# Optimization experiments

Hardware: AMD Instinct MI355X
Metric: run time of the kernel (lower is better)

The kernel has to match this reference:

```python
import jax, jax.numpy as jnp
import numpy as np


def setup_inputs() -> dict:
    key = jax.random.key(0)
    k1, k2 = jax.random.split(key)
    B, T, C = 16, 4096, 1024
    x = jax.random.normal(k1, (B, T, C), dtype=jnp.float32)
    raw = jax.random.normal(k2, (C,), dtype=jnp.float32)
    return {"x": x, "raw": raw}


def reference(x, raw):
    # x: [B, T, C]; raw: [C] learnable logits -> alpha = sigmoid(raw)
    a = jax.nn.sigmoid(raw)            # [C]
    one_minus_a = 1.0 - a
    y0 = x[:, 0, :]                     # y_0 = x_0 (original initializes with raw first step)

    def step(y_prev, x_t):
        y_t = a * x_t + one_minus_a * y_prev
        return y_t, y_t

    xs = jnp.moveaxis(x[:, 1:, :], 1, 0)   # [T-1, B, C], scan over time
    _, ys = jax.lax.scan(step, y0, xs)      # ys: [T-1, B, C]
    y = jnp.concatenate([y0[:, None, :], jnp.moveaxis(ys, 0, 1)], axis=1)  # [B, T, C]
    return y
```

## Files before the change

### kernel.cpp

```cpp
#include <hip/hip_runtime.h>
#include <math.h>


#define T_DIM 4096
#define C_DIM 1024
#define CG    64
#define NWAVE 16
#define LSUB  16
#define TILE_T (NWAVE * LSUB)
#define NTILES (T_DIM / TILE_T)

__global__ __launch_bounds__(1024, 1)
void ema_scan_kernel(const float* __restrict__ x,
                     const float* __restrict__ raw,
                     float* __restrict__ y) {
    __shared__ float carry_lds[NWAVE][CG];

    const int lane = threadIdx.x & (CG - 1);
    const int w    = threadIdx.x >> 6;
    const int cg   = blockIdx.x;
    const int b    = blockIdx.y;
    const int c    = cg * CG + lane;

    const float rv = raw[c];
    const float a  = 1.0f / (1.0f + expf(-rv));
    const float d  = 1.0f - a;
    const float d2 = d * d, d4 = d2 * d2, d8 = d4 * d4;
    const float d16 = d8 * d8;

    const size_t base = ((size_t)b * T_DIM) * (size_t)C_DIM + (size_t)c;

    float run = 0.0f;

    for (int tile = 0; tile < NTILES; ++tile) {
        const int t0 = tile * TILE_T + w * LSUB;
        const float* xp = x + base + (size_t)t0 * C_DIM;

        float xv[LSUB];
        #pragma unroll
        for (int i = 0; i < LSUB; ++i) xv[i] = xp[(size_t)i * C_DIM];

        float yl[LSUB];
        float s = 0.0f;
        if (tile == 0 && w == 0) {
            s = xv[0];
            yl[0] = s;
            #pragma unroll
            for (int i = 1; i < LSUB; ++i) { s = fmaf(a, xv[i], d * s); yl[i] = s; }
        } else {
            #pragma unroll
            for (int i = 0; i < LSUB; ++i) { s = fmaf(a, xv[i], d * s); yl[i] = s; }
        }

        carry_lds[w][lane] = s;
        __syncthreads();

        float acc = run;
        float cin = 0.0f;
        #pragma unroll
        for (int j = 0; j < NWAVE; ++j) {
            if (j == w) cin = acc;
            acc = fmaf(d16, acc, carry_lds[j][lane]);
        }
        run = acc;
        __syncthreads();

        float* yp = y + base + (size_t)t0 * C_DIM;
        float f = d;
        #pragma unroll
        for (int i = 0; i < LSUB; ++i) {
            yp[(size_t)i * C_DIM] = fmaf(f, cin, yl[i]);
            f *= d;
        }
    }
}

extern "C" void kernel_launch(void* const* d_in, const int* in_sizes, int n_in,
                              void* d_out, int out_size, void* d_ws, size_t ws_size,
                              hipStream_t stream) {
    const float* x   = (const float*)d_in[0];
    const float* raw = (const float*)d_in[1];
    float* y = (float*)d_out;

    dim3 grid(C_DIM / CG, 16);
    dim3 block(1024);
    ema_scan_kernel<<<grid, block, 0, stream>>>(x, raw, y);
}
```

Baseline: 442.1 us.

## Vectorize EMA scan with float4 and double-buffer tile loads across iterations

Threads now process four channels each with float4 loads and stores, and blocks shrink to 256 threads over 32 channels, which gives 512 blocks instead of 256. The next tile's loads are issued before the barrier, and the carry buffer in shared memory alternates between two slots so only one barrier is needed per tile. The intent is to raise memory-level parallelism and cut synchronization on a bandwidth-bound scan. In exchange the sequential carry chain grows to 32 rows per tile, and holding three float4 arrays raises register pressure.

```diff
diff --git a/kernel.cpp b/kernel.cpp
--- a/kernel.cpp
+++ b/kernel.cpp
@@ -2,77 +2,107 @@
 #include <math.h>
 
 
-#define T_DIM 4096
-#define C_DIM 1024
-#define CG    64
-#define NWAVE 16
-#define LSUB  16
-#define TILE_T (NWAVE * LSUB)
+#define B_DIM  16
+#define T_DIM  4096
+#define C_DIM  1024
+#define CG     32
+#define COLS   8
+#define NROW   32
+#define LSUB   8
+#define TILE_T (NROW * LSUB)
 #define NTILES (T_DIM / TILE_T)
+#define TSTR   (C_DIM / 4)
 
-__global__ __launch_bounds__(1024, 1)
+__device__ __forceinline__ float4 f4mul(float4 a, float4 b) {
+    float4 r; r.x = a.x*b.x; r.y = a.y*b.y; r.z = a.z*b.z; r.w = a.w*b.w; return r;
+}
+__device__ __forceinline__ float4 f4fma(float4 a, float4 b, float4 c) {
+    float4 r;
+    r.x = fmaf(a.x, b.x, c.x); r.y = fmaf(a.y, b.y, c.y);
+    r.z = fmaf(a.z, b.z, c.z); r.w = fmaf(a.w, b.w, c.w); return r;
+}
+
+__global__ __launch_bounds__(256, 2)
 void ema_scan_kernel(const float* __restrict__ x,
                      const float* __restrict__ raw,
                      float* __restrict__ y) {
-    __shared__ float carry_lds[NWAVE][CG];
+    __shared__ float4 carry[2][NROW][COLS];
 
-    const int lane = threadIdx.x & (CG - 1);
-    const int w    = threadIdx.x >> 6;
-    const int cg   = blockIdx.x;
-    const int b    = blockIdx.y;
-    const int c    = cg * CG + lane;
+    const int tid = threadIdx.x;
+    const int col = tid & (COLS - 1);
+    const int row = tid >> 3;
+    const int cg  = blockIdx.x;
+    const int b   = blockIdx.y;
+    const int c0  = cg * CG + col * 4;
 
-    const float rv = raw[c];
-    const float a  = 1.0f / (1.0f + expf(-rv));
-    const float d  = 1.0f - a;
-    const float d2 = d * d, d4 = d2 * d2, d8 = d4 * d4;
-    const float d16 = d8 * d8;
+    const float4 rv = *reinterpret_cast<const float4*>(raw + c0);
+    float4 a, d, d8;
+    a.x = 1.0f / (1.0f + expf(-rv.x));
+    a.y = 1.0f / (1.0f + expf(-rv.y));
+    a.z = 1.0f / (1.0f + expf(-rv.z));
+    a.w = 1.0f / (1.0f + expf(-rv.w));
+    d.x = 1.0f - a.x; d.y = 1.0f - a.y; d.z = 1.0f - a.z; d.w = 1.0f - a.w;
+    float4 d2 = f4mul(d, d), d4 = f4mul(d2, d2);
+    d8 = f4mul(d4, d4);
 
-    const size_t base = ((size_t)b * T_DIM) * (size_t)C_DIM + (size_t)c;
+    const size_t chanBase = ((size_t)b * T_DIM) * C_DIM + (size_t)c0;
+    const float4* xb = reinterpret_cast<const float4*>(x + chanBase);
+    float4*       yb = reinterpret_cast<float4*>(y + chanBase);
 
-    float run = 0.0f;
+    float4 run = {0.f, 0.f, 0.f, 0.f};
+    float4 xvA[LSUB], xvB[LSUB], yl[LSUB];
 
-    for (int tile = 0; tile < NTILES; ++tile) {
-        const int t0 = tile * TILE_T + w * LSUB;
-        const float* xp = x + base + (size_t)t0 * C_DIM;
+#define LOADT(XV, tt) {                                                        \
+    const float4* p = xb + (size_t)((tt) * TILE_T + row * LSUB) * TSTR;        \
+    _Pragma("unroll")                                                          \
+    for (int i = 0; i < LSUB; ++i) XV[i] = p[(size_t)i * TSTR]; }
 
-        float xv[LSUB];
-        #pragma unroll
-        for (int i = 0; i < LSUB; ++i) xv[i] = xp[(size_t)i * C_DIM];
+#define BODY(XC, XN, tt, pb, doload) {                                         \
+                   \
+    float4 s;                                                                  \
+    if ((tt) == 0 && row == 0) {                                               \
+        s = XC[0]; yl[0] = s;                 \
+        _Pragma("unroll")                                                      \
+        for (int i = 1; i < LSUB; ++i) { s = f4fma(d, s, f4mul(a, XC[i])); yl[i] = s; } \
+    } else {                                                                   \
+        s.x = s.y = s.z = s.w = 0.f;                                           \
+        _Pragma("unroll")                                                      \
+        for (int i = 0; i < LSUB; ++i) { s = f4fma(d, s, f4mul(a, XC[i])); yl[i] = s; } \
+    }                                                                          \
+                                                 \
+    carry[pb][row][col] = s;                                                   \
+     \
+    if (doload) LOADT(XN, (tt) + 1);                                           \
+       \
+    asm volatile("s_waitcnt lgkmcnt(0)" ::: "memory");                         \
+    __builtin_amdgcn_s_barrier();                                              \
+    asm volatile("" ::: "memory");                                             \
+                \
+    float4 acc = run;                                                          \
+    float4 cin = {0.f, 0.f, 0.f, 0.f};                                         \
+    _Pragma("unroll 8")                                                        \
+    for (int j = 0; j < NROW; ++j) {                                           \
+        float4 cj = carry[pb][j][col];                                         \
+        if (j == row) cin = acc;                                               \
+        acc = f4fma(d8, acc, cj);                                              \
+    }                                                                          \
+    run = acc;                                                                 \
+                     \
+    float4* q = yb + (size_t)((tt) * TILE_T + row * LSUB) * TSTR;              \
+    float4 f = d;                                                              \
+    _Pragma("unroll")                                                          \
+    for (int i = 0; i < LSUB; ++i) {                                           \
+        q[(size_t)i * TSTR] = f4fma(f, cin, yl[i]);                            \
+        f = f4mul(f, d);                                                       \
+    } }
 
-        float yl[LSUB];
-        float s = 0.0f;
-        if (tile == 0 && w == 0) {
-            s = xv[0];
-            yl[0] = s;
-            #pragma unroll
-            for (int i = 1; i < LSUB; ++i) { s = fmaf(a, xv[i], d * s); yl[i] = s; }
-        } else {
-            #pragma unroll
-            for (int i = 0; i < LSUB; ++i) { s = fmaf(a, xv[i], d * s); yl[i] = s; }
-        }
-
-        carry_lds[w][lane] = s;
-        __syncthreads();
-
-        float acc = run;
-        float cin = 0.0f;
-        #pragma unroll
-        for (int j = 0; j < NWAVE; ++j) {
-            if (j == w) cin = acc;
-            acc = fmaf(d16, acc, carry_lds[j][lane]);
-        }
-        run = acc;
-        __syncthreads();
-
-        float* yp = y + base + (size_t)t0 * C_DIM;
-        float f = d;
-        #pragma unroll
-        for (int i = 0; i < LSUB; ++i) {
-            yp[(size_t)i * C_DIM] = fmaf(f, cin, yl[i]);
-            f *= d;
-        }
+    LOADT(xvA, 0);
+    for (int tp = 0; tp < NTILES; tp += 2) {
+        BODY(xvA, xvB, tp,     0, true);
+        BODY(xvB, xvA, tp + 1, 1, (tp + 2 < NTILES));
     }
+#undef LOADT
+#undef BODY
 }
 
 extern "C" void kernel_launch(void* const* d_in, const int* in_sizes, int n_in,
@@ -82,7 +112,7 @@
     const float* raw = (const float*)d_in[1];
     float* y = (float*)d_out;
 
-    dim3 grid(C_DIM / CG, 16);
-    dim3 block(1024);
+    dim3 grid(C_DIM / CG, B_DIM);
+    dim3 block(NROW * COLS);
     ema_scan_kernel<<<grid, block, 0, stream>>>(x, raw, y);
 }
```

Result: slower. 456.2 us (+3.2%).
